# Performance work log

Hardware: AMD Instinct MI355X
Metric: run time of the kernel (lower is better)

Reference implementation:

```python
import jax, jax.numpy as jnp
import numpy as np

B, LP, LQ, D = 32, 2048, 512, 256

def setup_inputs() -> dict:
    key = jax.random.key(0)
    k1, k2, k3, k4 = jax.random.split(key, 4)
    x = jax.random.normal(k1, (B, LP, D), dtype=jnp.float32)
    y = jax.random.normal(k2, (B, LQ, D), dtype=jnp.float32)
    # nn.Linear(input_size, input_size): weight [D, D], bias [D]
    bound = 1.0 / np.sqrt(D)
    W = jax.random.uniform(k3, (D, D), minval=-bound, maxval=bound, dtype=jnp.float32)
    b = jax.random.uniform(k4, (D,), minval=-bound, maxval=bound, dtype=jnp.float32)
    return {"x": x, "y": y, "W": W, "b": b}

def reference(x, y, W, b):
    # shared linear + relu projection (torch Linear: x @ W.T + b)
    x_proj = jax.nn.relu(jnp.einsum('bpd,ed->bpe', x, W) + b)  # [B, LP, D]
    y_proj = jax.nn.relu(jnp.einsum('bqd,ed->bqe', y, W) + b)  # [B, LQ, D]
    # unscaled cross-attention scores
    scores = jnp.einsum('bpd,bqd->bpq', x_proj, y_proj)        # [B, LP, LQ]
    alpha = jax.nn.softmax(scores, axis=-1)
    # weighted sum over original (unprojected) y
    match_seq = jnp.einsum('bpq,bqd->bpd', alpha, y)           # [B, LP, D]
    return match_seq
```

## Files before the change

kernel.cpp:

```cpp
#include <hip/hip_runtime.h>
#include <stdint.h>

#define B_  32
#define LP_ 2048
#define LQ_ 512
#define D_  256

typedef __attribute__((ext_vector_type(8))) short short8;
typedef __attribute__((ext_vector_type(8))) _Float16 f16x8;
typedef __attribute__((ext_vector_type(4))) float f32x4;

__device__ __forceinline__ ushort f2h(float x) {
    union { _Float16 h; ushort u; } v;
    v.h = (_Float16)x;
    return v.u;
}
__device__ __forceinline__ void gl_lds16(const void* g, void* l) {
    __builtin_amdgcn_global_load_lds(
        (const __attribute__((address_space(1))) void*)g,
        (__attribute__((address_space(3))) void*)l, 16, 0, 0);
}


__global__ void k_prep(const float* __restrict__ W, const float* __restrict__ y,
                       ushort* __restrict__ Whf, ushort* __restrict__ yf) {
    __shared__ float t[32 * 260];
    if (blockIdx.x < 256) {
        int i = blockIdx.x * 256 + threadIdx.x;
        int e = i >> 8, k = i & 255;
        size_t off = (size_t)((k >> 5) * 16 + (e >> 4)) * 512 +
                     ((k >> 3) & 3) * 128 + (e & 15) * 8 + (k & 7);
        Whf[off] = f2h(W[i]);
        return;
    }
    int bid = blockIdx.x - 256;
    int b = bid >> 4, qc = bid & 15;
    int tid = threadIdx.x;
    int ql = tid >> 3;
    int d0 = (tid & 7) * 4;
#pragma unroll
    for (int p = 0; p < 8; p++) {
        int d = p * 32 + d0;
        float4 v = *(const float4*)(y + ((size_t)(b * LQ_ + qc * 32 + ql) * 256 + d));
        t[ql * 260 + d + 0] = v.x; t[ql * 260 + d + 1] = v.y;
        t[ql * 260 + d + 2] = v.z; t[ql * 260 + d + 3] = v.w;
    }
    __syncthreads();
    int w = tid >> 6, L = tid & 63, c = L & 15, quad = L >> 4;
#pragma unroll
    for (int ii = 0; ii < 4; ii++) {
        int nt = w * 4 + ii;
        short8 o;
#pragma unroll
        for (int j = 0; j < 8; j++)
            o[j] = (short)f2h(t[(quad * 8 + j) * 260 + nt * 16 + c]);
        *(short8*)(yf + ((size_t)(b * 256 + qc * 16 + nt) * 512 + L * 8)) = o;
    }
}

__global__ __launch_bounds__(256, 3) void k_proj(const float* __restrict__ y,
                                                 const ushort* __restrict__ Whf,
                                                 const float* __restrict__ bias,
                                                 ushort* __restrict__ Oy) {
    __shared__ __align__(16) ushort Ws[16704];
    const int tid  = threadIdx.x;
    const int w    = tid >> 6;
    const int L    = tid & 63;
    const int c    = L & 15;
    const int quad = L >> 4;
    const int row0 = blockIdx.x * 64 + w * 16;
    const int arow = row0 + c;

    f32x4 acc[16];
#pragma unroll
    for (int i = 0; i < 16; i++) acc[i] = (f32x4)0.f;

#define PSTAGE(kc, p)                                                          \
    {                                                                          \
        _Pragma("unroll")                                                      \
        for (int ii = 0; ii < 4; ii++) {                                       \
            int i = w * 4 + ii;                                                \
            gl_lds16(Whf + (size_t)(kc) * 8192 + i * 512 + L * 8,              \
                     (char*)Ws + (p) * 16384 + i * 1024);                      \
        }                                                                      \
    }

    PSTAGE(0, 0);
    float4 nx0 = *(const float4*)(y + (size_t)arow * 256 + quad * 8);
    float4 nx1 = *(const float4*)(y + (size_t)arow * 256 + quad * 8 + 4);

    for (int kc = 0; kc < 8; kc++) {
        __syncthreads();
        if (kc < 7) PSTAGE(kc + 1, (kc + 1) & 1);
        float4 cx0 = nx0, cx1 = nx1;
        if (kc < 7) {
            nx0 = *(const float4*)(y + (size_t)arow * 256 + (kc + 1) * 32 + quad * 8);
            nx1 = *(const float4*)(y + (size_t)arow * 256 + (kc + 1) * 32 + quad * 8 + 4);
        }
        float xs[8] = {cx0.x, cx0.y, cx0.z, cx0.w, cx1.x, cx1.y, cx1.z, cx1.w};
        f16x8 ah;
#pragma unroll
        for (int j = 0; j < 8; j++) ah[j] = (_Float16)xs[j];
        const ushort* buf = Ws + (kc & 1) * 8192;
#pragma unroll
        for (int nt = 0; nt < 16; nt++) {
            f16x8 bh = *(const f16x8*)(buf + nt * 512 + L * 8);
            acc[nt] = __builtin_amdgcn_mfma_f32_16x16x32_f16(ah, bh, acc[nt], 0, 0, 0);
        }
    }

    __syncthreads();
    float* tr = (float*)Ws + w * (16 * 130);
    const int rt_g = row0 >> 4;
#pragma unroll
    for (int half = 0; half < 2; half++) {
#pragma unroll
        for (int nt8 = 0; nt8 < 8; nt8++) {
            int nt = half * 8 + nt8;
            float bv = bias[nt * 16 + c];
#pragma unroll
            for (int r = 0; r < 4; r++)
                tr[(quad * 4 + r) * 130 + nt8 * 16 + c] = fmaxf(acc[nt][r] + bv, 0.f);
        }
#pragma unroll
        for (int ec4 = 0; ec4 < 4; ec4++) {
            int ec = half * 4 + ec4;
            short8 hh;
#pragma unroll
            for (int j = 0; j < 8; j++)
                hh[j] = (short)f2h(tr[c * 130 + ec4 * 32 + quad * 8 + j]);
            size_t blk = (size_t)(rt_g >> 5) * 256 + ec * 32 + (rt_g & 31);
            *(short8*)(Oy + blk * 512 + L * 8) = hh;
        }
    }
}

__global__ __launch_bounds__(256, 4) void k_attn(const float* __restrict__ x,
                                                 const ushort* __restrict__ Whf,
                                                 const float* __restrict__ bias,
                                                 const ushort* __restrict__ ypf,
                                                 const ushort* __restrict__ yf,
                                                 float* __restrict__ out) {
    __shared__ __align__(16) ushort lds[16384];
    const int tid  = threadIdx.x;
    const int w    = tid >> 6;
    const int L    = tid & 63;
    const int c    = L & 15;
    const int quad = L >> 4;

    const int bid = blockIdx.x;
    const int jj  = bid >> 3;
    const int b   = (bid & 7) * 4 + (jj >> 6);
    const int mt  = jj & 63;
    const int m0  = mt * 32;

#pragma unroll
    for (int ii = 0; ii < 4; ii++) {
        int unit = w * 4 + ii;
        int rs = unit >> 3, kc = unit & 7;
        const float* xs = x + ((size_t)(b * LP_ + m0 + rs * 16 + c)) * 256 + kc * 32 + quad * 8;
        float4 v0 = *(const float4*)xs;
        float4 v1 = *(const float4*)(xs + 4);
        f16x8 h;
        h[0] = (_Float16)v0.x; h[1] = (_Float16)v0.y;
        h[2] = (_Float16)v0.z; h[3] = (_Float16)v0.w;
        h[4] = (_Float16)v1.x; h[5] = (_Float16)v1.y;
        h[6] = (_Float16)v1.z; h[7] = (_Float16)v1.w;
        *(f16x8*)(lds + unit * 512 + L * 8) = h;
    }
    __syncthreads();

    {
        const int prs = w & 1, peh = w >> 1;
        float bv[8];
#pragma unroll
        for (int ne = 0; ne < 8; ne++) bv[ne] = bias[(peh * 8 + ne) * 16 + c];
        f32x4 pacc[8];
#pragma unroll
        for (int ne = 0; ne < 8; ne++) pacc[ne] = (f32x4)0.f;
        for (int kc = 0; kc < 8; kc++) {
            f16x8 ah = *(const f16x8*)(lds + (prs * 8 + kc) * 512 + L * 8);
#pragma unroll
            for (int ne = 0; ne < 8; ne++) {
                f16x8 wb = *(const f16x8*)(Whf + ((size_t)(kc * 16 + peh * 8 + ne)) * 512 + L * 8);
                pacc[ne] = __builtin_amdgcn_mfma_f32_16x16x32_f16(ah, wb, pacc[ne], 0, 0, 0);
            }
        }
#pragma unroll
        for (int ne = 0; ne < 8; ne++) {
#pragma unroll
            for (int r = 0; r < 4; r++) {
                float v = fmaxf(pacc[ne][r] + bv[ne], 0.f);
                int off = 8192 + (prs * 8 + peh * 4 + (ne >> 1)) * 512 +
                          ((ne & 1) * 2 + (c >> 3)) * 128 + (quad * 4 + r) * 8 + (c & 7);
                lds[off] = f2h(v);
            }
        }
    }

    f32x4 sc[2][8];
#pragma unroll
    for (int rs = 0; rs < 2; rs++)
#pragma unroll
        for (int qt = 0; qt < 8; qt++) sc[rs][qt] = (f32x4)0.f;
    __syncthreads();

    const ushort* pf = lds + 8192;
    const ushort* yb = ypf + (size_t)b * 256 * 512;
    for (int kc = 0; kc < 8; kc++) {
        f16x8 ah0 = *(const f16x8*)(pf + kc * 512 + L * 8);
        f16x8 ah1 = *(const f16x8*)(pf + (8 + kc) * 512 + L * 8);
#pragma unroll
        for (int qt = 0; qt < 8; qt++) {
            f16x8 bh = *(const f16x8*)(yb + ((size_t)kc * 32 + w * 8 + qt) * 512 + L * 8);
            sc[0][qt] = __builtin_amdgcn_mfma_f32_16x16x32_f16(ah0, bh, sc[0][qt], 0, 0, 0);
            sc[1][qt] = __builtin_amdgcn_mfma_f32_16x16x32_f16(ah1, bh, sc[1][qt], 0, 0, 0);
        }
    }

    __syncthreads();
    float* red  = (float*)lds;
    float* red2 = red + 128;
    float inv[2][4];
#pragma unroll
    for (int rs = 0; rs < 2; rs++)
#pragma unroll
        for (int r = 0; r < 4; r++) {
            float pm = sc[rs][0][r];
#pragma unroll
            for (int qt = 1; qt < 8; qt++) pm = fmaxf(pm, sc[rs][qt][r]);
#pragma unroll
            for (int mask = 1; mask <= 8; mask <<= 1) pm = fmaxf(pm, __shfl_xor(pm, mask));
            if (c == 0) red[(rs * 16 + quad * 4 + r) * 4 + w] = pm;
        }
    __syncthreads();
#pragma unroll
    for (int rs = 0; rs < 2; rs++)
#pragma unroll
        for (int r = 0; r < 4; r++) {
            int row = rs * 16 + quad * 4 + r;
            float m = fmaxf(fmaxf(red[row * 4], red[row * 4 + 1]),
                            fmaxf(red[row * 4 + 2], red[row * 4 + 3]));
            float ps = 0.f;
#pragma unroll
            for (int qt = 0; qt < 8; qt++) {
                float e = __expf(sc[rs][qt][r] - m);
                sc[rs][qt][r] = e;
                ps += e;
            }
#pragma unroll
            for (int mask = 1; mask <= 8; mask <<= 1) ps += __shfl_xor(ps, mask);
            if (c == 0) red2[row * 4 + w] = ps;
        }
    __syncthreads();
#pragma unroll
    for (int rs = 0; rs < 2; rs++)
#pragma unroll
        for (int r = 0; r < 4; r++) {
            int row = rs * 16 + quad * 4 + r;
            inv[rs][r] = 1.f / (red2[row * 4] + red2[row * 4 + 1] +
                                red2[row * 4 + 2] + red2[row * 4 + 3]);
        }
    __syncthreads();

#pragma unroll
    for (int rs = 0; rs < 2; rs++)
#pragma unroll
        for (int r = 0; r < 4; r++) {
            int m_loc = rs * 16 + quad * 4 + r;
            int swz = m_loc & 7;
            float iv = inv[rs][r];
#pragma unroll
            for (int qt = 0; qt < 8; qt++) {
                int q = w * 128 + qt * 16 + c;
                lds[m_loc * 512 + (((q >> 3) ^ swz) << 3) + (c & 7)] = f2h(sc[rs][qt][r] * iv);
            }
        }
    __syncthreads();

    f32x4 o[2][4];
#pragma unroll
    for (int rs = 0; rs < 2; rs++)
#pragma unroll
        for (int dt = 0; dt < 4; dt++) o[rs][dt] = (f32x4)0.f;
    const int dh = w;
    const int swzA = c & 7;
    for (int kcq = 0; kcq < 16; kcq++) {
        int chunk = kcq * 4 + quad;
        f16x8 af0 = *(const f16x8*)(lds + c * 512 + ((chunk ^ swzA) << 3));
        f16x8 af1 = *(const f16x8*)(lds + (16 + c) * 512 + ((chunk ^ swzA) << 3));
        const ushort* ybf = yf + ((size_t)(b * 256 + kcq * 16 + dh * 4)) * 512;
#pragma unroll
        for (int dt = 0; dt < 4; dt++) {
            f16x8 bfr = *(const f16x8*)(ybf + dt * 512 + L * 8);
            o[0][dt] = __builtin_amdgcn_mfma_f32_16x16x32_f16(af0, bfr, o[0][dt], 0, 0, 0);
            o[1][dt] = __builtin_amdgcn_mfma_f32_16x16x32_f16(af1, bfr, o[1][dt], 0, 0, 0);
        }
    }

#pragma unroll
    for (int rs = 0; rs < 2; rs++)
#pragma unroll
        for (int dt = 0; dt < 4; dt++)
#pragma unroll
            for (int r = 0; r < 4; r++) {
                int row = rs * 16 + quad * 4 + r;
                out[(size_t)(b * LP_ + m0 + row) * 256 + dh * 64 + dt * 16 + c] =
                    o[rs][dt][r];
            }
}

extern "C" void kernel_launch(void* const* d_in, const int* in_sizes, int n_in,
                              void* d_out, int out_size, void* d_ws, size_t ws_size,
                              hipStream_t stream) {
    const float* x    = (const float*)d_in[0];
    const float* y    = (const float*)d_in[1];
    const float* W    = (const float*)d_in[2];
    const float* bias = (const float*)d_in[3];
    float* out = (float*)d_out;

    char* ws = (char*)d_ws;
    size_t off = 0;
    ushort* Whf = (ushort*)(ws + off); off += (size_t)D_ * D_ * 2;
    ushort* yfb = (ushort*)(ws + off); off += (size_t)B_ * D_ * LQ_ * 2;
    ushort* ypf = (ushort*)(ws + off); off += (size_t)B_ * LQ_ * D_ * 2;

    k_prep<<<768, 256, 0, stream>>>(W, y, Whf, yfb);
    k_proj<<<256, 256, 0, stream>>>(y, Whf, bias, ypf);
    k_attn<<<B_ * 64, 256, 0, stream>>>(x, Whf, bias, ypf, yfb, out);
}
```

Before: 203.0 us.

## Double attention row tile to 64 rows with 512-thread blocks

```diff
diff --git a/kernel.cpp b/kernel.cpp
--- a/kernel.cpp
+++ b/kernel.cpp
@@ -135,30 +135,32 @@
     }
 }
 
-__global__ __launch_bounds__(256, 4) void k_attn(const float* __restrict__ x,
+__global__ __launch_bounds__(512, 4) void k_attn(const float* __restrict__ x,
                                                  const ushort* __restrict__ Whf,
                                                  const float* __restrict__ bias,
                                                  const ushort* __restrict__ ypf,
                                                  const ushort* __restrict__ yf,
                                                  float* __restrict__ out) {
-    __shared__ __align__(16) ushort lds[16384];
+    __shared__ __align__(16) ushort lds[32768];
     const int tid  = threadIdx.x;
     const int w    = tid >> 6;
     const int L    = tid & 63;
     const int c    = L & 15;
     const int quad = L >> 4;
+    const int rh   = w >> 2;
+    const int qh   = w & 3;
 
     const int bid = blockIdx.x;
     const int jj  = bid >> 3;
-    const int b   = (bid & 7) * 4 + (jj >> 6);
-    const int mt  = jj & 63;
-    const int m0  = mt * 32;
+    const int b   = (bid & 7) * 4 + (jj >> 5);
+    const int mt  = jj & 31;
+    const int m0  = mt * 64;
 
 #pragma unroll
     for (int ii = 0; ii < 4; ii++) {
         int unit = w * 4 + ii;
-        int rs = unit >> 3, kc = unit & 7;
-        const float* xs = x + ((size_t)(b * LP_ + m0 + rs * 16 + c)) * 256 + kc * 32 + quad * 8;
+        int rsg = unit >> 3, kc = unit & 7;
+        const float* xs = x + ((size_t)(b * LP_ + m0 + rsg * 16 + c)) * 256 + kc * 32 + quad * 8;
         float4 v0 = *(const float4*)xs;
         float4 v1 = *(const float4*)(xs + 4);
         f16x8 h;
@@ -171,31 +173,38 @@
     __syncthreads();
 
     {
-        const int prs = w & 1, peh = w >> 1;
-        float bv[8];
-#pragma unroll
-        for (int ne = 0; ne < 8; ne++) bv[ne] = bias[(peh * 8 + ne) * 16 + c];
-        f32x4 pacc[8];
-#pragma unroll
-        for (int ne = 0; ne < 8; ne++) pacc[ne] = (f32x4)0.f;
+        float bv[2];
+#pragma unroll
+        for (int ne = 0; ne < 2; ne++) bv[ne] = bias[(w * 2 + ne) * 16 + c];
+        f32x4 pacc[4][2];
+#pragma unroll
+        for (int rsg = 0; rsg < 4; rsg++)
+#pragma unroll
+            for (int ne = 0; ne < 2; ne++) pacc[rsg][ne] = (f32x4)0.f;
         for (int kc = 0; kc < 8; kc++) {
-            f16x8 ah = *(const f16x8*)(lds + (prs * 8 + kc) * 512 + L * 8);
-#pragma unroll
-            for (int ne = 0; ne < 8; ne++) {
-                f16x8 wb = *(const f16x8*)(Whf + ((size_t)(kc * 16 + peh * 8 + ne)) * 512 + L * 8);
-                pacc[ne] = __builtin_amdgcn_mfma_f32_16x16x32_f16(ah, wb, pacc[ne], 0, 0, 0);
-            }
-        }
-#pragma unroll
-        for (int ne = 0; ne < 8; ne++) {
-#pragma unroll
-            for (int r = 0; r < 4; r++) {
-                float v = fmaxf(pacc[ne][r] + bv[ne], 0.f);
-                int off = 8192 + (prs * 8 + peh * 4 + (ne >> 1)) * 512 +
-                          ((ne & 1) * 2 + (c >> 3)) * 128 + (quad * 4 + r) * 8 + (c & 7);
-                lds[off] = f2h(v);
-            }
-        }
+            f16x8 wb[2];
+#pragma unroll
+            for (int ne = 0; ne < 2; ne++)
+                wb[ne] = *(const f16x8*)(Whf + ((size_t)(kc * 16 + w * 2 + ne)) * 512 + L * 8);
+#pragma unroll
+            for (int rsg = 0; rsg < 4; rsg++) {
+                f16x8 ah = *(const f16x8*)(lds + (rsg * 8 + kc) * 512 + L * 8);
+                pacc[rsg][0] = __builtin_amdgcn_mfma_f32_16x16x32_f16(ah, wb[0], pacc[rsg][0], 0, 0, 0);
+                pacc[rsg][1] = __builtin_amdgcn_mfma_f32_16x16x32_f16(ah, wb[1], pacc[rsg][1], 0, 0, 0);
+            }
+        }
+#pragma unroll
+        for (int rsg = 0; rsg < 4; rsg++)
+#pragma unroll
+            for (int ne = 0; ne < 2; ne++) {
+#pragma unroll
+                for (int r = 0; r < 4; r++) {
+                    float v = fmaxf(pacc[rsg][ne][r] + bv[ne], 0.f);
+                    int off = 16384 + (rsg * 8 + w) * 512 +
+                              (ne * 2 + (c >> 3)) * 128 + (quad * 4 + r) * 8 + (c & 7);
+                    lds[off] = f2h(v);
+                }
+            }
     }
 
     f32x4 sc[2][8];
@@ -205,14 +214,14 @@
         for (int qt = 0; qt < 8; qt++) sc[rs][qt] = (f32x4)0.f;
     __syncthreads();
 
-    const ushort* pf = lds + 8192;
+    const ushort* pf = lds + 16384;
     const ushort* yb = ypf + (size_t)b * 256 * 512;
     for (int kc = 0; kc < 8; kc++) {
-        f16x8 ah0 = *(const f16x8*)(pf + kc * 512 + L * 8);
-        f16x8 ah1 = *(const f16x8*)(pf + (8 + kc) * 512 + L * 8);
+        f16x8 ah0 = *(const f16x8*)(pf + ((2 * rh) * 8 + kc) * 512 + L * 8);
+        f16x8 ah1 = *(const f16x8*)(pf + ((2 * rh + 1) * 8 + kc) * 512 + L * 8);
 #pragma unroll
         for (int qt = 0; qt < 8; qt++) {
-            f16x8 bh = *(const f16x8*)(yb + ((size_t)kc * 32 + w * 8 + qt) * 512 + L * 8);
+            f16x8 bh = *(const f16x8*)(yb + ((size_t)kc * 32 + qh * 8 + qt) * 512 + L * 8);
             sc[0][qt] = __builtin_amdgcn_mfma_f32_16x16x32_f16(ah0, bh, sc[0][qt], 0, 0, 0);
             sc[1][qt] = __builtin_amdgcn_mfma_f32_16x16x32_f16(ah1, bh, sc[1][qt], 0, 0, 0);
         }
@@ -220,7 +229,7 @@
 
     __syncthreads();
     float* red  = (float*)lds;
-    float* red2 = red + 128;
+    float* red2 = red + 256;
     float inv[2][4];
 #pragma unroll
     for (int rs = 0; rs < 2; rs++)
@@ -231,14 +240,14 @@
             for (int qt = 1; qt < 8; qt++) pm = fmaxf(pm, sc[rs][qt][r]);
 #pragma unroll
             for (int mask = 1; mask <= 8; mask <<= 1) pm = fmaxf(pm, __shfl_xor(pm, mask));
-            if (c == 0) red[(rs * 16 + quad * 4 + r) * 4 + w] = pm;
+            if (c == 0) red[(rh * 32 + rs * 16 + quad * 4 + r) * 4 + qh] = pm;
         }
     __syncthreads();
 #pragma unroll
     for (int rs = 0; rs < 2; rs++)
 #pragma unroll
         for (int r = 0; r < 4; r++) {
-            int row = rs * 16 + quad * 4 + r;
+            int row = rh * 32 + rs * 16 + quad * 4 + r;
             float m = fmaxf(fmaxf(red[row * 4], red[row * 4 + 1]),
                             fmaxf(red[row * 4 + 2], red[row * 4 + 3]));
             float ps = 0.f;
@@ -250,14 +259,14 @@
             }
 #pragma unroll
             for (int mask = 1; mask <= 8; mask <<= 1) ps += __shfl_xor(ps, mask);
-            if (c == 0) red2[row * 4 + w] = ps;
+            if (c == 0) red2[row * 4 + qh] = ps;
         }
     __syncthreads();
 #pragma unroll
     for (int rs = 0; rs < 2; rs++)
 #pragma unroll
         for (int r = 0; r < 4; r++) {
-            int row = rs * 16 + quad * 4 + r;
+            int row = rh * 32 + rs * 16 + quad * 4 + r;
             inv[rs][r] = 1.f / (red2[row * 4] + red2[row * 4 + 1] +
                                 red2[row * 4 + 2] + red2[row * 4 + 3]);
         }
@@ -267,12 +276,12 @@
     for (int rs = 0; rs < 2; rs++)
 #pragma unroll
         for (int r = 0; r < 4; r++) {
-            int m_loc = rs * 16 + quad * 4 + r;
+            int m_loc = rh * 32 + rs * 16 + quad * 4 + r;
             int swz = m_loc & 7;
             float iv = inv[rs][r];
 #pragma unroll
             for (int qt = 0; qt < 8; qt++) {
-                int q = w * 128 + qt * 16 + c;
+                int q = qh * 128 + qt * 16 + c;
                 lds[m_loc * 512 + (((q >> 3) ^ swz) << 3) + (c & 7)] = f2h(sc[rs][qt][r] * iv);
             }
         }
@@ -283,13 +292,12 @@
     for (int rs = 0; rs < 2; rs++)
 #pragma unroll
         for (int dt = 0; dt < 4; dt++) o[rs][dt] = (f32x4)0.f;
-    const int dh = w;
     const int swzA = c & 7;
     for (int kcq = 0; kcq < 16; kcq++) {
         int chunk = kcq * 4 + quad;
-        f16x8 af0 = *(const f16x8*)(lds + c * 512 + ((chunk ^ swzA) << 3));
-        f16x8 af1 = *(const f16x8*)(lds + (16 + c) * 512 + ((chunk ^ swzA) << 3));
-        const ushort* ybf = yf + ((size_t)(b * 256 + kcq * 16 + dh * 4)) * 512;
+        f16x8 af0 = *(const f16x8*)(lds + ((rh * 2) * 16 + c) * 512 + ((chunk ^ swzA) << 3));
+        f16x8 af1 = *(const f16x8*)(lds + ((rh * 2 + 1) * 16 + c) * 512 + ((chunk ^ swzA) << 3));
+        const ushort* ybf = yf + ((size_t)(b * 256 + kcq * 16 + qh * 4)) * 512;
 #pragma unroll
         for (int dt = 0; dt < 4; dt++) {
             f16x8 bfr = *(const f16x8*)(ybf + dt * 512 + L * 8);
@@ -304,8 +312,8 @@
         for (int dt = 0; dt < 4; dt++)
 #pragma unroll
             for (int r = 0; r < 4; r++) {
-                int row = rs * 16 + quad * 4 + r;
-                out[(size_t)(b * LP_ + m0 + row) * 256 + dh * 64 + dt * 16 + c] =
+                int row = (rh * 2 + rs) * 16 + quad * 4 + r;
+                out[(size_t)(b * LP_ + m0 + row) * 256 + qh * 64 + dt * 16 + c] =
                     o[rs][dt][r];
             }
 }
@@ -327,5 +335,5 @@
 
     k_prep<<<768, 256, 0, stream>>>(W, y, Whf, yfb);
     k_proj<<<256, 256, 0, stream>>>(y, Whf, bias, ypf);
-    k_attn<<<B_ * 64, 256, 0, stream>>>(x, Whf, bias, ypf, yfb, out);
-}
+    k_attn<<<B_ * 32, 512, 0, stream>>>(x, Whf, bias, ypf, yfb, out);
+}
```

Measured after the change: 206.5 us. No clear change (+1.8%).
